# Optimization experiments

Hardware: AMD Instinct MI355X
Metric: run time of the kernel (lower is better)

Reference implementation:

```python
import jax, jax.numpy as jnp
import numpy as np

DN = ('NCHW', 'OIHW', 'NCHW')

def _conv(x, w, padding):
    return jax.lax.conv_general_dilated(
        x, w, window_strides=(1, 1), padding=padding,
        dimension_numbers=DN)

def setup_inputs() -> dict:
    key = jax.random.key(0)
    k1, k2, k3, k4, k5 = jax.random.split(key, 5)
    nf = 40
    x = jax.random.normal(k1, (16, nf, 256, 256), dtype=jnp.float32)
    # PyTorch conv default init scale ~ 1/sqrt(fan_in)
    w2 = jax.random.normal(k2, (nf, nf, 1, 1), dtype=jnp.float32) / np.sqrt(nf)
    b2 = jax.random.normal(k3, (nf,), dtype=jnp.float32) * 0.01
    w3 = jax.random.normal(k4, (nf, nf, 3, 3), dtype=jnp.float32) / np.sqrt(nf * 9)
    w4 = jax.random.normal(k5, (nf, nf, 3, 3), dtype=jnp.float32) / np.sqrt(nf * 9)
    return {"x": x, "w2": w2, "b2": b2, "w3": w3, "w4": w4}

def reference(x, w2, b2, w3, w4):
    # k2: 1x1 conv + bias, then sigmoid gate (pixel attention)
    y = _conv(x, w2, padding='VALID') + b2[None, :, None, None]
    y = jax.nn.sigmoid(y)
    # k3: 3x3 conv (pad 1, no bias), gated elementwise
    out = _conv(x, w3, padding=((1, 1), (1, 1))) * y
    # k4: 3x3 conv (pad 1, no bias)
    out = _conv(out, w4, padding=((1, 1), (1, 1)))
    return out
```

## Files before the change

### kernel.cpp

```cpp
#include <hip/hip_runtime.h>
#include <hip/hip_bf16.h>

typedef __bf16 bf16;
typedef __bf16 bf16x2 __attribute__((ext_vector_type(2)));
typedef __bf16 bf16x4 __attribute__((ext_vector_type(4)));
typedef __bf16 bf16x8 __attribute__((ext_vector_type(8)));
typedef float f32x4 __attribute__((ext_vector_type(4)));

#define NF 40
#define HW 256
#define KPAD 384
#define MPAD 48

#define ZROW_ELEM_OFF (2 * MPAD * KPAD + MPAD * 64)
#define GATED_ELEM_OFF 40960
#define IMG_ELEMS ((size_t)16 * HW * HW * NF)
#define XT_ELEM_OFF (GATED_ELEM_OFF + IMG_ELEMS)
#define WS_SPLIT ((GATED_ELEM_OFF + IMG_ELEMS) * 2)
#define WS_FULL  ((GATED_ELEM_OFF + 2 * IMG_ELEMS) * 2)

#define RW 34
#define RU 612
#define GS 4904

__global__ void prep_weights(const float* __restrict__ w2,
                             const float* __restrict__ w3,
                             const float* __restrict__ w4,
                             bf16* __restrict__ ws) {
  int i = blockIdx.x * 256 + threadIdx.x;
  const int T = MPAD * KPAD;
  if (i < T) {
    int co = i / KPAD, k = i % KPAD;
    float v3 = 0.f, v4 = 0.f;
    if (co < NF && k < 360) {
      int tap = k / NF, ci = k - tap * NF;
      int ky = tap / 3, kx = tap - ky * 3;
      int idx = ((co * NF + ci) * 3 + ky) * 3 + kx;
      v3 = w3[idx];
      v4 = w4[idx];
    }
    ws[i] = (bf16)v3;
    ws[T + i] = (bf16)v4;
  }
  if (i < MPAD * 64) {
    int co = i / 64, ci = i - co * 64;
    float v = 0.f;
    if (co < NF && ci < NF) v = w2[co * NF + ci];
    ws[2 * T + i] = (bf16)v;
  }
  if (i < 1024) ws[ZROW_ELEM_OFF + i] = (bf16)0.f;
}

__global__ __launch_bounds__(256, 8)
void transpose_nhwc(const float* __restrict__ x, bf16* __restrict__ xT) {
  __shared__ bf16 xs[5 * 2056];
  const int tid = threadIdx.x;
  const int row = blockIdx.x;
  const int n   = blockIdx.y;
  const size_t nb = (size_t)n * NF * HW * HW + (size_t)row * HW;

#pragma unroll
  for (int cc = 0; cc < 10; ++cc) {
    bf16x4 v;
#pragma unroll
    for (int j = 0; j < 4; ++j)
      v[j] = (bf16)x[nb + (size_t)(cc * 4 + j) * HW * HW + tid];
    *(bf16x4*)&xs[(cc >> 1) * 2056 + tid * 8 + (cc & 1) * 4] = v;
  }
  __syncthreads();

  const size_t ob = ((size_t)n * HW * HW + (size_t)row * HW) * NF;
#pragma unroll
  for (int k = 0; k < 10; ++k) {
    int u = tid + k * 256;
    int px = u / 10, c4 = u - px * 10;
    bf16x4 v = *(const bf16x4*)&xs[(c4 >> 1) * 2056 + px * 8 + (c4 & 1) * 4];
    *(bf16x4*)&xT[ob + (size_t)u * 4] = v;
  }
}

__global__ __launch_bounds__(512, 4)
void k1_gate(const bf16* __restrict__ xT, const float* __restrict__ b2,
             const bf16* __restrict__ ws, bf16* __restrict__ gated) {
  __shared__ bf16 xs[5 * GS];

  const int tid  = threadIdx.x;
  const int lane = tid & 63;
  const int wid  = tid >> 6;
  const int l15  = lane & 15;
  const int lk   = lane >> 4;
  const int n    = blockIdx.z;
  const int X0   = blockIdx.x * 32;
  const int Y0   = blockIdx.y * 16;

  const bf16* W3A  = ws;
  const bf16* W2A  = ws + 2 * MPAD * KPAD;
  const bf16* zrow = ws + ZROW_ELEM_OFF;

  const bf16* bn = xT + (size_t)n * HW * HW * NF;
#pragma unroll
  for (int it = 0; it < 6; ++it) {
    int u = tid + it * 512;
    if (u < 5 * RU) {
      int c   = u / RU;
      int rem = u - c * RU;
      int r   = rem / RW;
      int p   = rem - r * RW;
      int gy  = Y0 - 1 + r, gx = X0 - 1 + p;
      bool ok = ((unsigned)gy < HW) && ((unsigned)gx < HW);
      int idx = ok ? (gy * HW + gx) : 0;
      const bf16* src = ok ? (bn + (size_t)idx * NF + c * 8) : zrow;
      bf16x8 v = *(const bf16x8*)src;
      *(bf16x8*)&xs[c * GS + rem * 8] = v;
    }
  }

  int gp3[12];
#pragma unroll
  for (int kk = 0; kk < 12; ++kk) {
    int k0 = kk * 32 + lk * 8;
    int kc = (k0 < 360) ? k0 : 0;
    int tap = kc / NF, ci0 = kc - tap * NF;
    int ky = tap / 3, kx = tap - ky * 3;
    gp3[kk] = (ci0 >> 3) * GS + (ky * RW + kx) * 8;
  }
  int gctr[2];
#pragma unroll
  for (int kk = 0; kk < 2; ++kk) {
    int k0 = kk * 32 + lk * 8;
    int ci0 = (k0 < NF) ? k0 : 0;
    gctr[kk] = (ci0 >> 3) * GS + (RW + 1) * 8;
  }
  int pb[4];
#pragma unroll
  for (int g = 0; g < 4; ++g) {
    int prow = wid * 2 + (g >> 1);
    int pcol = (g & 1) * 16 + l15;
    pb[g] = (prow * RW + pcol) * 8;
  }
  float b2v[3][4];
#pragma unroll
  for (int mt = 0; mt < 3; ++mt)
#pragma unroll
    for (int r = 0; r < 4; ++r) {
      int co = mt * 16 + lk * 4 + r;
      b2v[mt][r] = (co < NF) ? b2[co] : 0.f;
    }
  bf16x8 a2[2][3];
#pragma unroll
  for (int kk = 0; kk < 2; ++kk)
#pragma unroll
    for (int mt = 0; mt < 3; ++mt)
      a2[kk][mt] = *(const bf16x8*)&W2A[(mt * 16 + l15) * 64 + kk * 32 + lk * 8];

  __syncthreads();

  bf16x4 gv[4][3];
  {
    f32x4 g[4][3];
#pragma unroll
    for (int q = 0; q < 4; ++q)
#pragma unroll
      for (int mt = 0; mt < 3; ++mt) g[q][mt] = f32x4{0, 0, 0, 0};
#pragma unroll
    for (int kk = 0; kk < 2; ++kk)
#pragma unroll
      for (int q = 0; q < 4; ++q) {
        bf16x8 b = *(const bf16x8*)&xs[gctr[kk] + pb[q]];
#pragma unroll
        for (int mt = 0; mt < 3; ++mt)
          g[q][mt] = __builtin_amdgcn_mfma_f32_16x16x32_bf16(a2[kk][mt], b, g[q][mt], 0, 0, 0);
      }
#pragma unroll
    for (int q = 0; q < 4; ++q)
#pragma unroll
      for (int mt = 0; mt < 3; ++mt)
#pragma unroll
        for (int r = 0; r < 4; ++r)
          gv[q][mt][r] = (bf16)(1.f / (1.f + __expf(-(g[q][mt][r] + b2v[mt][r]))));
  }

  f32x4 f[4][3];
#pragma unroll
  for (int q = 0; q < 4; ++q)
#pragma unroll
    for (int mt = 0; mt < 3; ++mt) f[q][mt] = f32x4{0, 0, 0, 0};

#pragma unroll
  for (int kk = 0; kk < 12; ++kk) {
    bf16x8 a[3];
#pragma unroll
    for (int mt = 0; mt < 3; ++mt)
      a[mt] = *(const bf16x8*)&W3A[(mt * 16 + l15) * KPAD + kk * 32 + lk * 8];
#pragma unroll
    for (int q = 0; q < 4; ++q) {
      bf16x8 b = *(const bf16x8*)&xs[gp3[kk] + pb[q]];
#pragma unroll
      for (int mt = 0; mt < 3; ++mt)
        f[q][mt] = __builtin_amdgcn_mfma_f32_16x16x32_bf16(a[mt], b, f[q][mt], 0, 0, 0);
    }
  }

#pragma unroll
  for (int q = 0; q < 4; ++q) {
    int prow = wid * 2 + (q >> 1);
    int pcol = (q & 1) * 16 + l15;
    size_t gb = ((size_t)n * HW * HW + (size_t)(Y0 + prow) * HW + (X0 + pcol)) * NF;
#pragma unroll
    for (int mt = 0; mt < 3; ++mt) {
      int co0 = mt * 16 + lk * 4;
      if (co0 < NF) {
        bf16x4 ov;
#pragma unroll
        for (int r = 0; r < 4; ++r)
          ov[r] = (bf16)(f[q][mt][r] * (float)gv[q][mt][r]);
        *(bf16x4*)&gated[gb + co0] = ov;
      }
    }
  }
}

__global__ __launch_bounds__(512, 4)
void k2_conv(const bf16* __restrict__ gated, const bf16* __restrict__ ws,
             float* __restrict__ out) {
  __shared__ bf16 xs[5 * GS];

  const int tid  = threadIdx.x;
  const int lane = tid & 63;
  const int wid  = tid >> 6;
  const int l15  = lane & 15;
  const int lk   = lane >> 4;
  const int n    = blockIdx.z;
  const int X0   = blockIdx.x * 32;
  const int Y0   = blockIdx.y * 16;

  const bf16* W4A  = ws + MPAD * KPAD;
  const bf16* zrow = ws + ZROW_ELEM_OFF;

  const bf16* bn = gated + (size_t)n * HW * HW * NF;
#pragma unroll
  for (int it = 0; it < 6; ++it) {
    int u = tid + it * 512;
    if (u < 5 * RU) {
      int c   = u / RU;
      int rem = u - c * RU;
      int r   = rem / RW;
      int p   = rem - r * RW;
      int gy  = Y0 - 1 + r, gx = X0 - 1 + p;
      bool ok = ((unsigned)gy < HW) && ((unsigned)gx < HW);
      int idx = ok ? (gy * HW + gx) : 0;
      const bf16* src = ok ? (bn + (size_t)idx * NF + c * 8) : zrow;
      bf16x8 v = *(const bf16x8*)src;
      *(bf16x8*)&xs[c * GS + rem * 8] = v;
    }
  }

  int gp4[12];
#pragma unroll
  for (int kk = 0; kk < 12; ++kk) {
    int k0 = kk * 32 + lk * 8;
    int kc = (k0 < 360) ? k0 : 0;
    int tap = kc / NF, ci0 = kc - tap * NF;
    int ky = tap / 3, kx = tap - ky * 3;
    gp4[kk] = (ci0 >> 3) * GS + (ky * RW + kx) * 8;
  }
  int pb[4];
#pragma unroll
  for (int g = 0; g < 4; ++g) {
    int prow = wid * 2 + (g >> 1);
    int pcol = (g & 1) * 16 + l15;
    pb[g] = (prow * RW + pcol) * 8;
  }

  __syncthreads();

  f32x4 f[4][3];
#pragma unroll
  for (int q = 0; q < 4; ++q)
#pragma unroll
    for (int mt = 0; mt < 3; ++mt) f[q][mt] = f32x4{0, 0, 0, 0};

#pragma unroll
  for (int kk = 0; kk < 12; ++kk) {
    bf16x8 a[3];
#pragma unroll
    for (int mt = 0; mt < 3; ++mt)
      a[mt] = *(const bf16x8*)&W4A[(mt * 16 + l15) * KPAD + kk * 32 + lk * 8];
#pragma unroll
    for (int q = 0; q < 4; ++q) {
      bf16x8 b = *(const bf16x8*)&xs[gp4[kk] + pb[q]];
#pragma unroll
      for (int mt = 0; mt < 3; ++mt)
        f[q][mt] = __builtin_amdgcn_mfma_f32_16x16x32_bf16(a[mt], b, f[q][mt], 0, 0, 0);
    }
  }

  float* on = out + (size_t)n * NF * HW * HW;
#pragma unroll
  for (int q = 0; q < 4; ++q) {
    int prow = wid * 2 + (q >> 1);
    int pcol = (q & 1) * 16 + l15;
    float* orow = on + (size_t)(Y0 + prow) * HW + (X0 + pcol);
#pragma unroll
    for (int mt = 0; mt < 3; ++mt)
#pragma unroll
      for (int r = 0; r < 4; ++r) {
        int co = mt * 16 + lk * 4 + r;
        if (co < NF)
          orow[(size_t)co * HW * HW] = f[q][mt][r];
      }
  }
}

#define K1_RW 18
__global__ __launch_bounds__(512, 6)
void k1_gate_nchw(const float* __restrict__ x, const float* __restrict__ b2,
                  const bf16* __restrict__ ws, bf16* __restrict__ gated) {
  __shared__ bf16 xs[K1_RW * K1_RW * NF];

  const int tid  = threadIdx.x;
  const int lane = tid & 63;
  const int wid  = tid >> 6;
  const int l15  = lane & 15;
  const int lk   = lane >> 4;
  const int n    = blockIdx.z;
  const int X0   = blockIdx.x * 16;
  const int Y0   = blockIdx.y * 16;

  const bf16* W3A = ws;
  const bf16* W2A = ws + 2 * MPAD * KPAD;

  const float* xn = x + (size_t)n * NF * HW * HW;
  for (int i = tid; i < K1_RW * K1_RW * NF / 2; i += 512) {
    int cih = i / (K1_RW * K1_RW);
    int rem = i - cih * (K1_RW * K1_RW);
    int ci  = cih * 2;
    int yy  = rem / K1_RW, xx = rem - yy * K1_RW;
    int gy  = Y0 - 1 + yy, gx = X0 - 1 + xx;
    float v0 = 0.f, v1 = 0.f;
    if ((unsigned)gy < HW && (unsigned)gx < HW) {
      const float* p = xn + (size_t)ci * HW * HW + gy * HW + gx;
      v0 = p[0];
      v1 = p[HW * HW];
    }
    bf16x2 pr; pr[0] = (bf16)v0; pr[1] = (bf16)v1;
    *(bf16x2*)&xs[rem * NF + ci] = pr;
  }

  int off3[12];
#pragma unroll
  for (int kk = 0; kk < 12; ++kk) {
    int k0 = kk * 32 + lk * 8;
    int kc = (k0 < 360) ? k0 : 0;
    int tap = kc / NF, ci0 = kc - tap * NF;
    int ky = tap / 3, kx = tap - ky * 3;
    off3[kk] = (ky * K1_RW + kx) * NF + ci0;
  }
  int pb[2];
#pragma unroll
  for (int t2 = 0; t2 < 2; ++t2) {
    int pix = (wid * 2 + t2) * 16 + l15;
    int py = pix >> 4, px = pix & 15;
    pb[t2] = (py * K1_RW + px) * NF;
  }
  float b2v[3][4];
#pragma unroll
  for (int mt = 0; mt < 3; ++mt)
#pragma unroll
    for (int r = 0; r < 4; ++r) {
      int co = mt * 16 + lk * 4 + r;
      b2v[mt][r] = (co < NF) ? b2[co] : 0.f;
    }

  __syncthreads();

  bf16x4 gv[2][3];
  {
    f32x4 g[2][3];
#pragma unroll
    for (int t2 = 0; t2 < 2; ++t2)
#pragma unroll
      for (int mt = 0; mt < 3; ++mt) g[t2][mt] = f32x4{0, 0, 0, 0};
#pragma unroll
    for (int kk = 0; kk < 2; ++kk) {
      int k0 = kk * 32 + lk * 8;
      int goff = (K1_RW + 1) * NF + ((k0 < NF) ? k0 : 0);
      bf16x8 a[3];
#pragma unroll
      for (int mt = 0; mt < 3; ++mt)
        a[mt] = *(const bf16x8*)&W2A[(mt * 16 + l15) * 64 + k0];
#pragma unroll
      for (int t2 = 0; t2 < 2; ++t2) {
        bf16x8 b = *(const bf16x8*)&xs[pb[t2] + goff];
#pragma unroll
        for (int mt = 0; mt < 3; ++mt)
          g[t2][mt] = __builtin_amdgcn_mfma_f32_16x16x32_bf16(a[mt], b, g[t2][mt], 0, 0, 0);
      }
    }
#pragma unroll
    for (int t2 = 0; t2 < 2; ++t2)
#pragma unroll
      for (int mt = 0; mt < 3; ++mt)
#pragma unroll
        for (int r = 0; r < 4; ++r)
          gv[t2][mt][r] = (bf16)(1.f / (1.f + __expf(-(g[t2][mt][r] + b2v[mt][r]))));
  }

  f32x4 facc[2][3];
#pragma unroll
  for (int t2 = 0; t2 < 2; ++t2)
#pragma unroll
    for (int mt = 0; mt < 3; ++mt) facc[t2][mt] = f32x4{0, 0, 0, 0};

#pragma unroll
  for (int kk = 0; kk < 12; ++kk) {
    bf16x8 a[3];
#pragma unroll
    for (int mt = 0; mt < 3; ++mt)
      a[mt] = *(const bf16x8*)&W3A[(mt * 16 + l15) * KPAD + kk * 32 + lk * 8];
#pragma unroll
    for (int t2 = 0; t2 < 2; ++t2) {
      bf16x8 b = *(const bf16x8*)&xs[pb[t2] + off3[kk]];
#pragma unroll
      for (int mt = 0; mt < 3; ++mt)
        facc[t2][mt] = __builtin_amdgcn_mfma_f32_16x16x32_bf16(a[mt], b, facc[t2][mt], 0, 0, 0);
    }
  }

#pragma unroll
  for (int t2 = 0; t2 < 2; ++t2) {
    int pix = (wid * 2 + t2) * 16 + l15;
    int py = pix >> 4, px = pix & 15;
    size_t base = ((size_t)n * HW * HW + (size_t)(Y0 + py) * HW + (X0 + px)) * NF;
#pragma unroll
    for (int mt = 0; mt < 3; ++mt) {
      int co0 = mt * 16 + lk * 4;
      if (co0 < NF) {
        bf16x4 ov;
#pragma unroll
        for (int r = 0; r < 4; ++r)
          ov[r] = (bf16)(facc[t2][mt][r] * (float)gv[t2][mt][r]);
        *(bf16x4*)&gated[base + co0] = ov;
      }
    }
  }
}

extern "C" void kernel_launch(void* const* d_in, const int* in_sizes, int n_in,
                              void* d_out, int out_size, void* d_ws, size_t ws_size,
                              hipStream_t stream) {
  const float* x  = (const float*)d_in[0];
  const float* w2 = (const float*)d_in[1];
  const float* b2 = (const float*)d_in[2];
  const float* w3 = (const float*)d_in[3];
  const float* w4 = (const float*)d_in[4];
  float* out = (float*)d_out;
  bf16* ws   = (bf16*)d_ws;

  hipLaunchKernelGGL(prep_weights, dim3(72), dim3(256), 0, stream, w2, w3, w4, ws);

  bf16* gated = ws + GATED_ELEM_OFF;
  if (ws_size >= WS_FULL) {
    bf16* xT = ws + XT_ELEM_OFF;
    hipLaunchKernelGGL(transpose_nhwc, dim3(256, 16), dim3(256), 0, stream, x, xT);
    hipLaunchKernelGGL(k1_gate, dim3(8, 16, 16), dim3(512), 0, stream,
                       xT, b2, ws, gated);
  } else {
    hipLaunchKernelGGL(k1_gate_nchw, dim3(16, 16, 16), dim3(512), 0, stream,
                       x, b2, ws, gated);
  }
  hipLaunchKernelGGL(k2_conv, dim3(8, 16, 16), dim3(512), 0, stream,
                     gated, ws, out);
}
```

Measured before the change: 312.4 us.

## Halve spatial tile height to 8 rows and widen gated stores via lane shuffle

Both conv kernels now use 32x8 pixel tiles with 256-thread blocks instead of 32x16 with 512 threads. This halves shared memory per block and raises the occupancy hint, at the cost of more halo reloading per output. The gated output in k1 is now written as 8-element bf16 vectors by exchanging halves between lanes with a shuffle. k2's output store loop is reordered so each thread writes its two column groups back to back.

```diff
diff --git a/kernel.cpp b/kernel.cpp
--- a/kernel.cpp
+++ b/kernel.cpp
@@ -16,12 +16,12 @@
 #define GATED_ELEM_OFF 40960
 #define IMG_ELEMS ((size_t)16 * HW * HW * NF)
 #define XT_ELEM_OFF (GATED_ELEM_OFF + IMG_ELEMS)
-#define WS_SPLIT ((GATED_ELEM_OFF + IMG_ELEMS) * 2)
 #define WS_FULL  ((GATED_ELEM_OFF + 2 * IMG_ELEMS) * 2)
 
-#define RW 34
-#define RU 612
-#define GS 4904
+#define RW2 34
+#define RH2 10
+#define RU2 340
+#define GSE 2720
 
 __global__ void prep_weights(const float* __restrict__ w2,
                              const float* __restrict__ w3,
@@ -79,10 +79,10 @@
   }
 }
 
-__global__ __launch_bounds__(512, 4)
-void k1_gate(const bf16* __restrict__ xT, const float* __restrict__ b2,
+__global__ __launch_bounds__(256, 6)
+void k1_tile(const bf16* __restrict__ xT, const float* __restrict__ b2,
              const bf16* __restrict__ ws, bf16* __restrict__ gated) {
-  __shared__ bf16 xs[5 * GS];
+  __shared__ bf16 xs[5 * GSE];
 
   const int tid  = threadIdx.x;
   const int lane = tid & 63;
@@ -91,7 +91,7 @@
   const int lk   = lane >> 4;
   const int n    = blockIdx.z;
   const int X0   = blockIdx.x * 32;
-  const int Y0   = blockIdx.y * 16;
+  const int Y0   = blockIdx.y * 8;
 
   const bf16* W3A  = ws;
   const bf16* W2A  = ws + 2 * MPAD * KPAD;
@@ -99,19 +99,17 @@
 
   const bf16* bn = xT + (size_t)n * HW * HW * NF;
 #pragma unroll
-  for (int it = 0; it < 6; ++it) {
-    int u = tid + it * 512;
-    if (u < 5 * RU) {
-      int c   = u / RU;
-      int rem = u - c * RU;
-      int r   = rem / RW;
-      int p   = rem - r * RW;
+  for (int it = 0; it < 7; ++it) {
+    int u = tid + it * 256;
+    if (u < 5 * RU2) {
+      int c   = u / RU2;
+      int rem = u - c * RU2;
+      int r   = rem / RW2;
+      int p   = rem - r * RW2;
       int gy  = Y0 - 1 + r, gx = X0 - 1 + p;
       bool ok = ((unsigned)gy < HW) && ((unsigned)gx < HW);
-      int idx = ok ? (gy * HW + gx) : 0;
-      const bf16* src = ok ? (bn + (size_t)idx * NF + c * 8) : zrow;
-      bf16x8 v = *(const bf16x8*)src;
-      *(bf16x8*)&xs[c * GS + rem * 8] = v;
+      const bf16* src = ok ? (bn + (size_t)(gy * HW + gx) * NF + c * 8) : zrow;
+      *(bf16x8*)&xs[u * 8] = *(const bf16x8*)src;
     }
   }
 
@@ -122,21 +120,21 @@
     int kc = (k0 < 360) ? k0 : 0;
     int tap = kc / NF, ci0 = kc - tap * NF;
     int ky = tap / 3, kx = tap - ky * 3;
-    gp3[kk] = (ci0 >> 3) * GS + (ky * RW + kx) * 8;
+    gp3[kk] = (ci0 >> 3) * GSE + (ky * RW2 + kx) * 8;
   }
   int gctr[2];
 #pragma unroll
   for (int kk = 0; kk < 2; ++kk) {
     int k0 = kk * 32 + lk * 8;
     int ci0 = (k0 < NF) ? k0 : 0;
-    gctr[kk] = (ci0 >> 3) * GS + (RW + 1) * 8;
+    gctr[kk] = (ci0 >> 3) * GSE + (RW2 + 1) * 8;
   }
   int pb[4];
 #pragma unroll
-  for (int g = 0; g < 4; ++g) {
-    int prow = wid * 2 + (g >> 1);
-    int pcol = (g & 1) * 16 + l15;
-    pb[g] = (prow * RW + pcol) * 8;
+  for (int q = 0; q < 4; ++q) {
+    int prow = wid * 2 + (q >> 1);
+    int pcol = (q & 1) * 16 + l15;
+    pb[q] = (prow * RW2 + pcol) * 8;
   }
   float b2v[3][4];
 #pragma unroll
@@ -208,22 +206,26 @@
     size_t gb = ((size_t)n * HW * HW + (size_t)(Y0 + prow) * HW + (X0 + pcol)) * NF;
 #pragma unroll
     for (int mt = 0; mt < 3; ++mt) {
+      union { bf16x4 v; unsigned long long u; } mine, part;
+#pragma unroll
+      for (int r = 0; r < 4; ++r)
+        mine.v[r] = (bf16)(f[q][mt][r] * (float)gv[q][mt][r]);
+      part.u = __shfl(mine.u, (lane + 16) & 63);
       int co0 = mt * 16 + lk * 4;
-      if (co0 < NF) {
-        bf16x4 ov;
-#pragma unroll
-        for (int r = 0; r < 4; ++r)
-          ov[r] = (bf16)(f[q][mt][r] * (float)gv[q][mt][r]);
-        *(bf16x4*)&gated[gb + co0] = ov;
+      if (((lk & 1) == 0) && (co0 < NF)) {
+        bf16x8 w;
+#pragma unroll
+        for (int r = 0; r < 4; ++r) { w[r] = mine.v[r]; w[r + 4] = part.v[r]; }
+        *(bf16x8*)&gated[gb + co0] = w;
       }
     }
   }
 }
 
-__global__ __launch_bounds__(512, 4)
-void k2_conv(const bf16* __restrict__ gated, const bf16* __restrict__ ws,
+__global__ __launch_bounds__(256, 6)
+void k2_tile(const bf16* __restrict__ gated, const bf16* __restrict__ ws,
              float* __restrict__ out) {
-  __shared__ bf16 xs[5 * GS];
+  __shared__ bf16 xs[5 * GSE];
 
   const int tid  = threadIdx.x;
   const int lane = tid & 63;
@@ -232,26 +234,24 @@
   const int lk   = lane >> 4;
   const int n    = blockIdx.z;
   const int X0   = blockIdx.x * 32;
-  const int Y0   = blockIdx.y * 16;
+  const int Y0   = blockIdx.y * 8;
 
   const bf16* W4A  = ws + MPAD * KPAD;
   const bf16* zrow = ws + ZROW_ELEM_OFF;
 
   const bf16* bn = gated + (size_t)n * HW * HW * NF;
 #pragma unroll
-  for (int it = 0; it < 6; ++it) {
-    int u = tid + it * 512;
-    if (u < 5 * RU) {
-      int c   = u / RU;
-      int rem = u - c * RU;
-      int r   = rem / RW;
-      int p   = rem - r * RW;
+  for (int it = 0; it < 7; ++it) {
+    int u = tid + it * 256;
+    if (u < 5 * RU2) {
+      int c   = u / RU2;
+      int rem = u - c * RU2;
+      int r   = rem / RW2;
+      int p   = rem - r * RW2;
       int gy  = Y0 - 1 + r, gx = X0 - 1 + p;
       bool ok = ((unsigned)gy < HW) && ((unsigned)gx < HW);
-      int idx = ok ? (gy * HW + gx) : 0;
-      const bf16* src = ok ? (bn + (size_t)idx * NF + c * 8) : zrow;
-      bf16x8 v = *(const bf16x8*)src;
-      *(bf16x8*)&xs[c * GS + rem * 8] = v;
+      const bf16* src = ok ? (bn + (size_t)(gy * HW + gx) * NF + c * 8) : zrow;
+      *(bf16x8*)&xs[u * 8] = *(const bf16x8*)src;
     }
   }
 
@@ -262,52 +262,54 @@
     int kc = (k0 < 360) ? k0 : 0;
     int tap = kc / NF, ci0 = kc - tap * NF;
     int ky = tap / 3, kx = tap - ky * 3;
-    gp4[kk] = (ci0 >> 3) * GS + (ky * RW + kx) * 8;
+    gp4[kk] = (ci0 >> 3) * GSE + (ky * RW2 + kx) * 8;
   }
   int pb[4];
-#pragma unroll
-  for (int g = 0; g < 4; ++g) {
-    int prow = wid * 2 + (g >> 1);
-    int pcol = (g & 1) * 16 + l15;
-    pb[g] = (prow * RW + pcol) * 8;
-  }
-
-  __syncthreads();
-
-  f32x4 f[4][3];
-#pragma unroll
-  for (int q = 0; q < 4; ++q)
-#pragma unroll
-    for (int mt = 0; mt < 3; ++mt) f[q][mt] = f32x4{0, 0, 0, 0};
-
-#pragma unroll
-  for (int kk = 0; kk < 12; ++kk) {
-    bf16x8 a[3];
-#pragma unroll
-    for (int mt = 0; mt < 3; ++mt)
-      a[mt] = *(const bf16x8*)&W4A[(mt * 16 + l15) * KPAD + kk * 32 + lk * 8];
-#pragma unroll
-    for (int q = 0; q < 4; ++q) {
-      bf16x8 b = *(const bf16x8*)&xs[gp4[kk] + pb[q]];
-#pragma unroll
-      for (int mt = 0; mt < 3; ++mt)
-        f[q][mt] = __builtin_amdgcn_mfma_f32_16x16x32_bf16(a[mt], b, f[q][mt], 0, 0, 0);
-    }
-  }
-
-  float* on = out + (size_t)n * NF * HW * HW;
 #pragma unroll
   for (int q = 0; q < 4; ++q) {
     int prow = wid * 2 + (q >> 1);
     int pcol = (q & 1) * 16 + l15;
-    float* orow = on + (size_t)(Y0 + prow) * HW + (X0 + pcol);
+    pb[q] = (prow * RW2 + pcol) * 8;
+  }
+
+  __syncthreads();
+
+  f32x4 f[4][3];
+#pragma unroll
+  for (int q = 0; q < 4; ++q)
+#pragma unroll
+    for (int mt = 0; mt < 3; ++mt) f[q][mt] = f32x4{0, 0, 0, 0};
+
+#pragma unroll
+  for (int kk = 0; kk < 12; ++kk) {
+    bf16x8 a[3];
+#pragma unroll
+    for (int mt = 0; mt < 3; ++mt)
+      a[mt] = *(const bf16x8*)&W4A[(mt * 16 + l15) * KPAD + kk * 32 + lk * 8];
+#pragma unroll
+    for (int q = 0; q < 4; ++q) {
+      bf16x8 b = *(const bf16x8*)&xs[gp4[kk] + pb[q]];
+#pragma unroll
+      for (int mt = 0; mt < 3; ++mt)
+        f[q][mt] = __builtin_amdgcn_mfma_f32_16x16x32_bf16(a[mt], b, f[q][mt], 0, 0, 0);
+    }
+  }
+
+  float* on = out + (size_t)n * NF * HW * HW;
+#pragma unroll
+  for (int qh = 0; qh < 2; ++qh) {
+    int prow = wid * 2 + qh;
+    float* orow = on + (size_t)(Y0 + prow) * HW + X0;
 #pragma unroll
     for (int mt = 0; mt < 3; ++mt)
 #pragma unroll
       for (int r = 0; r < 4; ++r) {
         int co = mt * 16 + lk * 4 + r;
-        if (co < NF)
-          orow[(size_t)co * HW * HW] = f[q][mt][r];
+        if (co < NF) {
+#pragma unroll
+          for (int ql = 0; ql < 2; ++ql)
+            orow[(size_t)co * HW * HW + ql * 16 + l15] = f[qh * 2 + ql][mt][r];
+        }
       }
   }
 }
@@ -463,12 +465,12 @@
   if (ws_size >= WS_FULL) {
     bf16* xT = ws + XT_ELEM_OFF;
     hipLaunchKernelGGL(transpose_nhwc, dim3(256, 16), dim3(256), 0, stream, x, xT);
-    hipLaunchKernelGGL(k1_gate, dim3(8, 16, 16), dim3(512), 0, stream,
+    hipLaunchKernelGGL(k1_tile, dim3(8, 32, 16), dim3(256), 0, stream,
                        xT, b2, ws, gated);
   } else {
     hipLaunchKernelGGL(k1_gate_nchw, dim3(16, 16, 16), dim3(512), 0, stream,
                        x, b2, ws, gated);
   }
-  hipLaunchKernelGGL(k2_conv, dim3(8, 16, 16), dim3(512), 0, stream,
+  hipLaunchKernelGGL(k2_tile, dim3(8, 32, 16), dim3(256), 0, stream,
                      gated, ws, out);
 }
```

Result: slower. 452.0 us (+44.7%).
